# Kernel optimization log

Hardware: AMD Instinct MI355X
Metric: run time of the kernel (lower is better)

Reference implementation:

```python
import jax, jax.numpy as jnp
import numpy as np

NUM_HEADS = 12  # per-branch heads = NUM_HEADS // 3 = 4


def setup_inputs() -> dict:
    key = jax.random.key(0)
    ks = jax.random.split(key, 11)
    B, N, C = 4, 2048, 768
    s = 0.02
    return {
        "x": jax.random.normal(ks[0], (B, N, C), jnp.float32),
        "Wqkv1": jax.random.normal(ks[1], (C, C), jnp.float32) * s,
        "Wqkv2": jax.random.normal(ks[2], (C, C), jnp.float32) * s,
        "Wqkv3": jax.random.normal(ks[3], (C, C), jnp.float32) * s,
        "Wp1": jax.random.normal(ks[4], (C // 3, C), jnp.float32) * s,
        "bp1": jax.random.normal(ks[5], (C,), jnp.float32) * s,
        "Wp2": jax.random.normal(ks[6], (C // 3, C), jnp.float32) * s,
        "bp2": jax.random.normal(ks[7], (C,), jnp.float32) * s,
        "Wp3": jax.random.normal(ks[8], (C // 3, C), jnp.float32) * s,
        "bp3": jax.random.normal(ks[9], (C,), jnp.float32) * s,
        "Wg": jax.random.normal(ks[10], (C, 3), jnp.float32) * s,
    }


def _branch(x, Wqkv, Wp, bp, B, N, C):
    Hb = NUM_HEADS // 3          # heads per branch
    hd = C // NUM_HEADS          # head dim
    scale = hd ** (-0.5)
    qkv = (x @ Wqkv).reshape(B, N, 3, Hb, hd)
    qkv = jnp.transpose(qkv, (2, 0, 3, 1, 4))  # [3, B, Hb, N, hd]
    q, k, v = qkv[0], qkv[1], qkv[2]
    attn = jax.nn.softmax(jnp.einsum('bhqd,bhkd->bhqk', q, k) * scale, axis=-1)
    o = jnp.einsum('bhqk,bhkd->bqhd', attn, v).reshape(B, N, C // 3)
    return o @ Wp + bp  # [B, N, C]


def _gate(z, Wg):
    prob_soft = jax.nn.softmax(z @ Wg, axis=-1)
    prob_hard = jax.nn.one_hot(jnp.argmax(prob_soft, axis=-1), 3, dtype=prob_soft.dtype)
    # straight-through estimator
    return jax.lax.stop_gradient(prob_hard - prob_soft) + prob_soft


def reference(x, Wqkv1, Wqkv2, Wqkv3, Wp1, bp1, Wp2, bp2, Wp3, bp3, Wg):
    B, N, C = x.shape
    prob_true = _gate(x, Wg)                                # [B, N, 3]
    x1 = _branch(x, Wqkv1, Wp1, bp1, B, N, C)
    x2 = _branch(x, Wqkv2, Wp2, bp2, B, N, C)
    x3 = _branch(x, Wqkv3, Wp3, bp3, B, N, C)
    # detached gate path (gate sees stop_gradient(x))
    prob_true_d = _gate(jax.lax.stop_gradient(x), Wg)
    xo = (x1 * prob_true[..., 0:1] + x2 * prob_true[..., 1:2]
          + x3 * prob_true[..., 2:3])
    sg = jax.lax.stop_gradient
    xd = (sg(x1) * prob_true_d[..., 0:1] + sg(x2) * prob_true_d[..., 1:2]
          + sg(x3) * prob_true_d[..., 2:3])
    idx = jnp.argmax(prob_true, axis=-1).reshape(-1, 1)
    return (xo, xd, idx)
```

## Files before the change

kernel.cpp:

```cpp
#include <hip/hip_runtime.h>

typedef short s16x4 __attribute__((ext_vector_type(4)));
typedef short s16x8 __attribute__((ext_vector_type(8)));
typedef float f32x4 __attribute__((ext_vector_type(4)));
typedef unsigned u32x4 __attribute__((ext_vector_type(4)));
typedef unsigned short u16;
typedef unsigned char u8;

__device__ __forceinline__ u16 f2b(float f) {
    union { float f; unsigned u; } v; v.f = f;
    unsigned r = v.u + 0x7FFFu + ((v.u >> 16) & 1u);
    return (u16)(r >> 16);
}

__device__ __forceinline__ float fexp2(float x) {
    float r; asm("v_exp_f32 %0, %1" : "=v"(r) : "v"(x)); return r;
}

__device__ __forceinline__ unsigned cvtpk(float lo, float hi) {
    unsigned r; asm("v_cvt_pk_bf16_f32 %0, %1, %2" : "=v"(r) : "v"(lo), "v"(hi)); return r;
}

__device__ __forceinline__ void GLL(const void* g, void* l) {
    __builtin_amdgcn_global_load_lds(
        (const __attribute__((address_space(1))) unsigned int*)g,
        (__attribute__((address_space(3))) unsigned int*)l, 16, 0, 0);
}

__device__ __forceinline__ void vmwait0() {
    asm volatile("s_waitcnt vmcnt(0)" ::: "memory");
    __builtin_amdgcn_sched_barrier(0);
}

#define QSCALE 0.1803368801111244f

__global__ __launch_bounds__(256) void prolog_kernel(const float* __restrict__ x,
                                                     const float* __restrict__ Wg,
                                                     u16* __restrict__ xb,
                                                     u8* __restrict__ kArr,
                                                     float* __restrict__ out,
                                                     const float* __restrict__ W0,
                                                     const float* __restrict__ W1,
                                                     const float* __restrict__ W2,
                                                     const float* __restrict__ W3,
                                                     const float* __restrict__ W4,
                                                     const float* __restrict__ W5,
                                                     u16* __restrict__ wqt,
                                                     u16* __restrict__ wpt) {
    __shared__ u16 tile[32][34];
    if (blockIdx.x < 2048) {
        int t = blockIdx.x * 4 + (threadIdx.x >> 6);
        int lane = threadIdx.x & 63;
        const float* xr = x + (size_t)t * 768;
        u16* xw = xb + (size_t)t * 768;
        float z0 = 0.f, z1 = 0.f, z2 = 0.f;
        #pragma unroll
        for (int s = 0; s < 3; s++) {
            int base = s * 256 + lane * 4;
            f32x4 v = *(const f32x4*)(xr + base);
            s16x4 o;
            #pragma unroll
            for (int j = 0; j < 4; j++) {
                o[j] = (short)f2b(v[j]);
                z0 = fmaf(v[j], Wg[(base + j) * 3 + 0], z0);
                z1 = fmaf(v[j], Wg[(base + j) * 3 + 1], z1);
                z2 = fmaf(v[j], Wg[(base + j) * 3 + 2], z2);
            }
            *(s16x4*)(xw + base) = o;
        }
        for (int o = 32; o; o >>= 1) {
            z0 += __shfl_xor(z0, o);
            z1 += __shfl_xor(z1, o);
            z2 += __shfl_xor(z2, o);
        }
        if (lane == 0) {
            int k = 0; float b = z0;
            if (z1 > b) { b = z1; k = 1; }
            if (z2 > b) { b = z2; k = 2; }
            out[12582912 + t] = (float)k;
            kArr[t] = (u8)k;
        }
    } else {
        int wb = blockIdx.x - 2048;
        int y, bt;
        if (wb < 1728) { y = wb / 576; bt = wb % 576; }
        else           { int w2 = wb - 1728; y = 3 + w2 / 192; bt = w2 % 192; }
        const float* W; u16* dst; int K;
        if (y < 3) { W = (y == 0) ? W0 : (y == 1) ? W1 : W2; dst = wqt + y * 589824; K = 768; }
        else       { W = (y == 3) ? W3 : (y == 4) ? W4 : W5; dst = wpt + (y - 3) * 196608; K = 256; }
        int ktiles = K >> 5;
        int kt = bt % ktiles, nt = bt / ktiles;
        int tx = threadIdx.x & 31, ty = threadIdx.x >> 5;
        #pragma unroll
        for (int i = 0; i < 4; i++) {
            int k = kt * 32 + ty + i * 8;
            tile[ty + i * 8][tx] = f2b(W[(size_t)k * 768 + nt * 32 + tx]);
        }
        __syncthreads();
        #pragma unroll
        for (int i = 0; i < 4; i++) {
            int n = nt * 32 + ty + i * 8;
            dst[(size_t)n * K + kt * 32 + tx] = tile[tx][ty + i * 8];
        }
    }
}

__global__ __launch_bounds__(64) void compact_kernel(const u8* __restrict__ kArr,
                                                     u16* __restrict__ perm,
                                                     int* __restrict__ cnt,
                                                     int* __restrict__ startA) {
    int batch = blockIdx.x;
    int lane = threadIdx.x;
    const u8* ka = kArr + batch * 2048;
    u8 kv[32];
    #pragma unroll
    for (int i = 0; i < 32; i++) kv[i] = ka[i * 64 + lane];
    u16* pm = perm + batch * 2048;
    int off = 0;
    for (int br = 0; br < 3; br++) {
        int c = 0;
        #pragma unroll
        for (int i = 0; i < 32; i++) {
            bool p = (kv[i] == (u8)br);
            unsigned long long m = __ballot(p);
            int rank = __popcll(m & ((1ull << lane) - 1ull));
            if (p) pm[off + c + rank] = (u16)(i * 64 + lane);
            c += __popcll(m);
        }
        if (lane == 0) { cnt[br * 4 + batch] = c; startA[br * 4 + batch] = off; }
        off += c;
    }
}

__global__ __launch_bounds__(256) void qkv_gemm_kernel(const u16* __restrict__ A,
                                                       const u16* __restrict__ Bt_all,
                                                       const u16* __restrict__ perm,
                                                       const int* __restrict__ cnt,
                                                       const int* __restrict__ startA,
                                                       u16* __restrict__ Qo,
                                                       u16* __restrict__ Ko,
                                                       u16* __restrict__ Vt) {
    __shared__ u16 As[128 * 64];
    __shared__ u16 Bs[128 * 64];
    const int tid = threadIdx.x;
    const int lane = tid & 63, w = tid >> 6, wm = w >> 1, wn = w & 1;
    const int g = lane >> 4, c15 = lane & 15;
    const int cx = c15 & 7;
    const int b = blockIdx.x;
    const int j = b >> 3;
    const int v = j % 18;
    const int branch = v / 6;
    const int m0 = ((b & 7) * 8 + j / 18) * 128;
    const int n0 = (v % 6) * 128;
    const u16* Bt = Bt_all + (size_t)branch * 589824;

    const int l8 = lane >> 3;
    const int ch = (lane & 7) ^ l8;
    const int batch0 = m0 >> 11, pbase = m0 & 2047;
    const u16* Arow[4];
    if (n0 < 256) {
        const int cb = branch * 4 + batch0;
        const int count = min(2048, cnt[cb]);
        if (pbase >= count) return;
        const u16* ci = perm + batch0 * 2048 + startA[cb];
        #pragma unroll
        for (int it = 0; it < 4; it++) {
            int slot = pbase + w * 32 + l8 + it * 8;
            int tok = ci[slot < count ? slot : count - 1] & 2047;
            Arow[it] = A + (size_t)(batch0 * 2048 + tok) * 768 + ch * 8;
        }
    } else {
        #pragma unroll
        for (int it = 0; it < 4; it++)
            Arow[it] = A + (size_t)(m0 + w * 32 + l8 + it * 8) * 768 + ch * 8;
    }
    const u16* Bsrc = Bt + (size_t)(n0 + w * 32 + l8) * 768 + ch * 8;
    u16* AsW = As + w * 2048;
    u16* BsW = Bs + w * 2048;

    f32x4 z4 = {0.f, 0.f, 0.f, 0.f};
    f32x4 acc[4][4];
    for (int mi = 0; mi < 4; mi++)
        for (int ni = 0; ni < 4; ni++) acc[mi][ni] = z4;

    for (int k0 = 0; k0 < 768; k0 += 64) {
        __syncthreads();
        #pragma unroll
        for (int it = 0; it < 4; it++) {
            GLL(Arow[it] + k0, AsW + it * 512);
            GLL(Bsrc + (size_t)(it * 8) * 768 + k0, BsW + it * 512);
        }
        vmwait0();
        __syncthreads();
        #pragma unroll
        for (int kk = 0; kk < 2; kk++) {
            s16x8 af[4], bf[4];
            #pragma unroll
            for (int i = 0; i < 4; i++) {
                af[i] = *(const s16x8*)&As[(wm * 64 + i * 16 + c15) * 64 + (((kk * 4 + g) ^ cx) * 8)];
                bf[i] = *(const s16x8*)&Bs[(wn * 64 + i * 16 + c15) * 64 + (((kk * 4 + g) ^ cx) * 8)];
            }
            for (int mi = 0; mi < 4; mi++)
                for (int ni = 0; ni < 4; ni++)
                    acc[mi][ni] = __builtin_amdgcn_mfma_f32_16x16x32_bf16(
                        af[mi], bf[ni], acc[mi][ni], 0, 0, 0);
        }
    }

    for (int mi = 0; mi < 4; mi++) {
        int r = m0 + wm * 64 + mi * 16 + g * 4;
        int batch = r >> 11, nbase = r & 2047;
        for (int ni = 0; ni < 4; ni++) {
            int cN = n0 + wn * 64 + ni * 16 + c15;
            int p = cN >> 8, h = (cN >> 6) & 3, d = cN & 63;
            size_t hb = (size_t)((branch * 4 + batch) * 4 + h) * 131072;
            f32x4 vv = acc[mi][ni];
            if (p == 2) {
                s16x4 pk;
                for (int rg = 0; rg < 4; rg++) pk[rg] = (short)f2b(vv[rg]);
                int pos = nbase & 31;
                int slot = ((pos & 15) >> 2) * 8 + ((pos >> 4) << 2);
                *(s16x4*)(Vt + hb + (size_t)d * 2048 + (nbase & ~31) + slot) = pk;
            } else if (p == 0) {
                for (int rg = 0; rg < 4; rg++)
                    Qo[hb + (size_t)(nbase + rg) * 64 + d] = f2b(vv[rg] * QSCALE);
            } else {
                for (int rg = 0; rg < 4; rg++)
                    Ko[hb + (size_t)(nbase + rg) * 64 + d] = f2b(vv[rg]);
            }
        }
    }
}

#define ATTN_STEP(KF, VF) do {                                                              \
    _Pragma("unroll")                                                                       \
    for (int s = 0; s < 2; s++) {                                                           \
        f32x4 sa0 = __builtin_amdgcn_mfma_f32_16x16x32_bf16(KF[0][0], qf[s][0], z4, 0, 0, 0); \
        sa0 = __builtin_amdgcn_mfma_f32_16x16x32_bf16(KF[0][1], qf[s][1], sa0, 0, 0, 0);    \
        f32x4 sa1 = __builtin_amdgcn_mfma_f32_16x16x32_bf16(KF[1][0], qf[s][0], z4, 0, 0, 0); \
        sa1 = __builtin_amdgcn_mfma_f32_16x16x32_bf16(KF[1][1], qf[s][1], sa1, 0, 0, 0);    \
        float q0 = fexp2(sa0[0]), q1 = fexp2(sa0[1]);                                       \
        float q2 = fexp2(sa0[2]), q3 = fexp2(sa0[3]);                                       \
        float q4 = fexp2(sa1[0]), q5 = fexp2(sa1[1]);                                       \
        float q6 = fexp2(sa1[2]), q7 = fexp2(sa1[3]);                                       \
        lsp[s] += ((q0 + q1) + (q2 + q3)) + ((q4 + q5) + (q6 + q7));                        \
        u32x4 pw;                                                                           \
        pw[0] = cvtpk(q0, q1); pw[1] = cvtpk(q2, q3);                                       \
        pw[2] = cvtpk(q4, q5); pw[3] = cvtpk(q6, q7);                                       \
        union { u32x4 w; s16x8 h; } pu; pu.w = pw;                                          \
        s16x8 pb = pu.h;                                                                    \
        _Pragma("unroll")                                                                   \
        for (int dt = 0; dt < 4; dt++)                                                      \
            oac[s][dt] = __builtin_amdgcn_mfma_f32_16x16x32_bf16(VF[dt], pb, oac[s][dt], 0, 0, 0); \
    }                                                                                       \
} while (0)

#define STAGE(B, T) do {                                                  \
    const unsigned char* _ks = Ksrc + (size_t)(T) * 8192;                 \
    const unsigned char* _vs = Vsrc + (size_t)(T) * 128;                  \
    unsigned char* _kd = &lds[(B) * 16384 + w * 2048];                    \
    unsigned char* _vd = &lds[(B) * 16384 + 8192 + w * 2048];             \
    GLL(_ks, _kd); GLL(_ks + 1024, _kd + 1024);                           \
    GLL(_vs, _vd); GLL(_vs + 32768, _vd + 1024);                          \
} while (0)

#define TILE_STEP(B) do {                                                               \
    const unsigned char* _KL = &lds[(B) * 16384];                                       \
    const unsigned char* _VL = &lds[(B) * 16384 + 8192];                                \
    s16x8 kf[2][2], vf[4];                                                              \
    _Pragma("unroll")                                                                   \
    for (int t = 0; t < 2; t++)                                                         \
        _Pragma("unroll")                                                               \
        for (int h = 0; h < 2; h++)                                                     \
            kf[t][h] = *(const s16x8*)(_KL + (t * 16 + c) * 128 + (((h * 4 + g) ^ cx) * 16)); \
    _Pragma("unroll")                                                                   \
    for (int dt = 0; dt < 4; dt++)                                                      \
        vf[dt] = *(const s16x8*)(_VL + (dt * 16 + c) * 128 + ((g ^ cx) * 16));          \
    ATTN_STEP(kf, vf);                                                                  \
    _Pragma("unroll")                                                                   \
    for (int t = 0; t < 2; t++)                                                         \
        _Pragma("unroll")                                                               \
        for (int h = 0; h < 2; h++)                                                     \
            kf[t][h] = *(const s16x8*)(_KL + ((t + 2) * 16 + c) * 128 + (((h * 4 + g) ^ cx) * 16)); \
    _Pragma("unroll")                                                                   \
    for (int dt = 0; dt < 4; dt++)                                                      \
        vf[dt] = *(const s16x8*)(_VL + (dt * 16 + c) * 128 + (((4 + g) ^ cx) * 16));    \
    ATTN_STEP(kf, vf);                                                                  \
} while (0)

__global__ __launch_bounds__(256, 4) void attn_kernel(const u16* __restrict__ Qg,
                                                      const u16* __restrict__ Kg,
                                                      const u16* __restrict__ Vg,
                                                      const int* __restrict__ cnt,
                                                      u16* __restrict__ Og) {
    __shared__ unsigned char lds[32768];
    const int tid = threadIdx.x;
    const int w = tid >> 6, lane = tid & 63;
    const int b = blockIdx.x;
    const int j = b >> 3;
    const int inst = (b & 7) * 6 + (j % 6);
    const int branch = inst >> 4, batch = (inst >> 2) & 3, h = inst & 3;
    const int cb = branch * 4 + batch;
    const int count = min(2048, cnt[cb]);
    const int qbase = (j / 6) * 128;
    if (qbase >= count) return;
    const int qt = (j / 6) * 4 + w;
    const int g = lane >> 4, c = lane & 15;
    const int cx = c & 7;
    const u16* Qh = Qg + (size_t)inst * 131072;

    f32x4 z4 = {0.f, 0.f, 0.f, 0.f};
    s16x8 qf[2][2];
    #pragma unroll
    for (int kk = 0; kk < 2; kk++) {
        qf[0][kk] = *(const s16x8*)(Qh + (size_t)(qt * 32 + c) * 64 + kk * 32 + g * 8);
        qf[1][kk] = *(const s16x8*)(Qh + (size_t)(qt * 32 + 16 + c) * 64 + kk * 32 + g * 8);
    }

    f32x4 oac[2][4];
    #pragma unroll
    for (int s = 0; s < 2; s++)
        #pragma unroll
        for (int dt = 0; dt < 4; dt++) oac[s][dt] = z4;
    float lsp[2] = {0.f, 0.f};

    const int swz = (((lane & 7) ^ ((lane >> 3) & 7)) << 4);
    const unsigned char* Ksrc = (const unsigned char*)(Kg + (size_t)inst * 131072)
                                + w * 2048 + ((lane >> 3) << 7) + swz;
    const unsigned char* Vsrc = (const unsigned char*)(Vg + (size_t)inst * 131072)
                                + (size_t)w * 65536 + ((lane >> 3) << 12) + swz;

    STAGE(0, 0);
    vmwait0();
    __syncthreads();
    for (int t2 = 0; t2 < 32; t2++) {
        int cur = t2 & 1;
        if (t2 + 1 < 32) STAGE(cur ^ 1, t2 + 1);
        TILE_STEP(cur);
        vmwait0();
        __syncthreads();
    }

    #pragma unroll
    for (int s = 0; s < 2; s++) {
        float ls = lsp[s];
        ls += __shfl_xor(ls, 16);
        ls += __shfl_xor(ls, 32);
        float inv = 1.0f / ls;
        int slot = qt * 32 + s * 16 + c;
        u16* dst = Og + ((size_t)cb * 2048 + slot) * 256 + h * 64;
        #pragma unroll
        for (int dt = 0; dt < 4; dt++) {
            s16x4 ob;
            for (int rg = 0; rg < 4; rg++) ob[rg] = (short)f2b(oac[s][dt][rg] * inv);
            *(s16x4*)(dst + dt * 16 + g * 4) = ob;
        }
    }
}

__global__ __launch_bounds__(256) void proj_gemm_kernel(const u16* __restrict__ Oall,
                                                        const u16* __restrict__ Wpt_all,
                                                        const u16* __restrict__ perm,
                                                        const int* __restrict__ cnt,
                                                        const int* __restrict__ startA,
                                                        const float* __restrict__ bp1,
                                                        const float* __restrict__ bp2,
                                                        const float* __restrict__ bp3,
                                                        float* __restrict__ out) {
    __shared__ u16 As[128 * 64];
    __shared__ u16 Bs[128 * 64];
    const int tid = threadIdx.x;
    const int lane = tid & 63, w = tid >> 6, wm = w >> 1, wn = w & 1;
    const int g = lane >> 4, c15 = lane & 15;
    const int cx = c15 & 7;
    const int branch = blockIdx.z;
    const int m0 = blockIdx.y * 128, n0 = blockIdx.x * 128;
    const int batch = m0 >> 11;
    const int cb = branch * 4 + batch;
    const int count = min(2048, cnt[cb]);
    const int pbase = m0 & 2047;
    if (pbase >= count) return;
    const u16* A = Oall + (size_t)branch * 8192 * 256;
    const u16* Bt = Wpt_all + (size_t)branch * 196608;
    const float* bp = (branch == 0) ? bp1 : ((branch == 1) ? bp2 : bp3);

    const int l8 = lane >> 3;
    const int ch = (lane & 7) ^ l8;
    const u16* Asrc = A + (size_t)(m0 + w * 32 + l8) * 256 + ch * 8;
    const u16* Bsrc = Bt + (size_t)(n0 + w * 32 + l8) * 256 + ch * 8;
    u16* AsW = As + w * 2048;
    u16* BsW = Bs + w * 2048;

    f32x4 z4 = {0.f, 0.f, 0.f, 0.f};
    f32x4 acc[4][4];
    for (int mi = 0; mi < 4; mi++)
        for (int ni = 0; ni < 4; ni++) acc[mi][ni] = z4;

    for (int k0 = 0; k0 < 256; k0 += 64) {
        __syncthreads();
        #pragma unroll
        for (int it = 0; it < 4; it++) {
            GLL(Asrc + (size_t)(it * 8) * 256 + k0, AsW + it * 512);
            GLL(Bsrc + (size_t)(it * 8) * 256 + k0, BsW + it * 512);
        }
        vmwait0();
        __syncthreads();
        #pragma unroll
        for (int kk = 0; kk < 2; kk++) {
            s16x8 af[4], bf[4];
            #pragma unroll
            for (int i = 0; i < 4; i++) {
                af[i] = *(const s16x8*)&As[(wm * 64 + i * 16 + c15) * 64 + (((kk * 4 + g) ^ cx) * 8)];
                bf[i] = *(const s16x8*)&Bs[(wn * 64 + i * 16 + c15) * 64 + (((kk * 4 + g) ^ cx) * 8)];
            }
            for (int mi = 0; mi < 4; mi++)
                for (int ni = 0; ni < 4; ni++)
                    acc[mi][ni] = __builtin_amdgcn_mfma_f32_16x16x32_bf16(
                        af[mi], bf[ni], acc[mi][ni], 0, 0, 0);
        }
    }

    const u16* ci = perm + batch * 2048 + startA[cb];
    for (int mi = 0; mi < 4; mi++) {
        int r = pbase + wm * 64 + mi * 16 + g * 4;
        for (int ni = 0; ni < 4; ni++) {
            int cN = n0 + wn * 64 + ni * 16 + c15;
            float bj = bp[cN];
            f32x4 v = acc[mi][ni];
            for (int rg = 0; rg < 4; rg++) {
                int slot = r + rg;
                if (slot < count) {
                    int t = batch * 2048 + (ci[slot] & 2047);
                    float wv = v[rg] + bj;
                    out[(size_t)t * 768 + cN] = wv;
                    out[6291456u + (size_t)t * 768 + cN] = wv;
                }
            }
        }
    }
}

extern "C" void kernel_launch(void* const* d_in, const int* in_sizes, int n_in,
                              void* d_out, int out_size, void* d_ws, size_t ws_size,
                              hipStream_t stream) {
    const float* x   = (const float*)d_in[0];
    const float* Wq1 = (const float*)d_in[1];
    const float* Wq2 = (const float*)d_in[2];
    const float* Wq3 = (const float*)d_in[3];
    const float* Wp1 = (const float*)d_in[4];
    const float* bp1 = (const float*)d_in[5];
    const float* Wp2 = (const float*)d_in[6];
    const float* bp2 = (const float*)d_in[7];
    const float* Wp3 = (const float*)d_in[8];
    const float* bp3 = (const float*)d_in[9];
    const float* Wg  = (const float*)d_in[10];
    float* out = (float*)d_out;

    char* ws = (char*)d_ws;
    u16* xb    = (u16*)(ws + 0);
    u16* wqt   = (u16*)(ws + 12582912);
    u16* wpt   = (u16*)(ws + 16121856);
    u16* Qb    = (u16*)(ws + 17301504);
    u16* Kb    = (u16*)(ws + 29884416);
    u16* Vtb   = (u16*)(ws + 42467328);
    u16* Ob    = (u16*)(ws + 55050240);
    u16* perm  = (u16*)(ws + 67633152);
    int* cnt   = (int*)(ws + 67649536);
    int* start = (int*)(ws + 67649600);
    u8*  kArr  = (u8*) (ws + 67649664);

    prolog_kernel<<<4352, 256, 0, stream>>>(x, Wg, xb, kArr, out,
                                            Wq1, Wq2, Wq3, Wp1, Wp2, Wp3, wqt, wpt);
    compact_kernel<<<4, 64, 0, stream>>>(kArr, perm, cnt, start);
    qkv_gemm_kernel<<<1152, 256, 0, stream>>>(xb, wqt, perm, cnt, start, Qb, Kb, Vtb);
    attn_kernel<<<768, 256, 0, stream>>>(Qb, Kb, Vtb, cnt, Ob);
    proj_gemm_kernel<<<dim3(6, 64, 3), 256, 0, stream>>>(Ob, wpt, perm, cnt, start, bp1, bp2, bp3, out);
}
```

Baseline: 124.8 us.

## Double-buffer QKV GEMM LDS tiles with K-step 32 to overlap loads

The QKV projection GEMM now uses two LDS buffers with a K-slice of 32 instead of a single buffer with a K-slice of 64. The next slice is issued via global_load_lds before the MFMAs on the current one run, so memory latency overlaps compute. The LDS swizzle and per-lane source addressing are reworked for the 32-wide rows. This doubles the number of barriers and gives each stage less MFMA work to hide a load behind.

```diff
diff --git a/kernel.cpp b/kernel.cpp
--- a/kernel.cpp
+++ b/kernel.cpp
@@ -132,6 +132,13 @@
     }
 }
 
+#define QKV_STAGE(BUF, K0) do {                              \
+    GLL(srcA0 + (K0), &As[BUF][w * 1024]);                   \
+    GLL(srcA1 + (K0), &As[BUF][w * 1024 + 512]);             \
+    GLL(srcB0 + (K0), &Bs[BUF][w * 1024]);                   \
+    GLL(srcB1 + (K0), &Bs[BUF][w * 1024 + 512]);             \
+} while (0)
+
 __global__ __launch_bounds__(256) void qkv_gemm_kernel(const u16* __restrict__ A,
                                                        const u16* __restrict__ Bt_all,
                                                        const u16* __restrict__ perm,
@@ -140,12 +147,12 @@
                                                        u16* __restrict__ Qo,
                                                        u16* __restrict__ Ko,
                                                        u16* __restrict__ Vt) {
-    __shared__ u16 As[128 * 64];
-    __shared__ u16 Bs[128 * 64];
+    __shared__ u16 As[2][4096];
+    __shared__ u16 Bs[2][4096];
     const int tid = threadIdx.x;
     const int lane = tid & 63, w = tid >> 6, wm = w >> 1, wn = w & 1;
     const int g = lane >> 4, c15 = lane & 15;
-    const int cx = c15 & 7;
+    const int cx2 = c15 & 3;
     const int b = blockIdx.x;
     const int j = b >> 3;
     const int v = j % 18;
@@ -154,57 +161,51 @@
     const int n0 = (v % 6) * 128;
     const u16* Bt = Bt_all + (size_t)branch * 589824;
 
-    const int l8 = lane >> 3;
-    const int ch = (lane & 7) ^ l8;
+    const int l4 = lane >> 2;
+    const int ch = (lane & 3) ^ (l4 & 3);
     const int batch0 = m0 >> 11, pbase = m0 & 2047;
-    const u16* Arow[4];
+    const u16 *srcA0, *srcA1;
     if (n0 < 256) {
         const int cb = branch * 4 + batch0;
         const int count = min(2048, cnt[cb]);
         if (pbase >= count) return;
         const u16* ci = perm + batch0 * 2048 + startA[cb];
-        #pragma unroll
-        for (int it = 0; it < 4; it++) {
-            int slot = pbase + w * 32 + l8 + it * 8;
-            int tok = ci[slot < count ? slot : count - 1] & 2047;
-            Arow[it] = A + (size_t)(batch0 * 2048 + tok) * 768 + ch * 8;
-        }
+        int s0 = pbase + w * 32 + l4;      if (s0 >= count) s0 = count - 1;
+        int s1 = pbase + w * 32 + 16 + l4; if (s1 >= count) s1 = count - 1;
+        srcA0 = A + (size_t)(batch0 * 2048 + (ci[s0] & 2047)) * 768 + ch * 8;
+        srcA1 = A + (size_t)(batch0 * 2048 + (ci[s1] & 2047)) * 768 + ch * 8;
     } else {
-        #pragma unroll
-        for (int it = 0; it < 4; it++)
-            Arow[it] = A + (size_t)(m0 + w * 32 + l8 + it * 8) * 768 + ch * 8;
-    }
-    const u16* Bsrc = Bt + (size_t)(n0 + w * 32 + l8) * 768 + ch * 8;
-    u16* AsW = As + w * 2048;
-    u16* BsW = Bs + w * 2048;
+        srcA0 = A + (size_t)(m0 + w * 32 + l4) * 768 + ch * 8;
+        srcA1 = A + (size_t)(m0 + w * 32 + 16 + l4) * 768 + ch * 8;
+    }
+    const u16* srcB0 = Bt + (size_t)(n0 + w * 32 + l4) * 768 + ch * 8;
+    const u16* srcB1 = Bt + (size_t)(n0 + w * 32 + 16 + l4) * 768 + ch * 8;
 
     f32x4 z4 = {0.f, 0.f, 0.f, 0.f};
     f32x4 acc[4][4];
     for (int mi = 0; mi < 4; mi++)
         for (int ni = 0; ni < 4; ni++) acc[mi][ni] = z4;
 
-    for (int k0 = 0; k0 < 768; k0 += 64) {
-        __syncthreads();
-        #pragma unroll
-        for (int it = 0; it < 4; it++) {
-            GLL(Arow[it] + k0, AsW + it * 512);
-            GLL(Bsrc + (size_t)(it * 8) * 768 + k0, BsW + it * 512);
-        }
-        vmwait0();
-        __syncthreads();
-        #pragma unroll
-        for (int kk = 0; kk < 2; kk++) {
+    QKV_STAGE(0, 0);
+    vmwait0();
+    __syncthreads();
+    for (int st = 0; st < 24; st++) {
+        int cur = st & 1;
+        if (st + 1 < 24) QKV_STAGE(cur ^ 1, (st + 1) * 32);
+        {
             s16x8 af[4], bf[4];
             #pragma unroll
             for (int i = 0; i < 4; i++) {
-                af[i] = *(const s16x8*)&As[(wm * 64 + i * 16 + c15) * 64 + (((kk * 4 + g) ^ cx) * 8)];
-                bf[i] = *(const s16x8*)&Bs[(wn * 64 + i * 16 + c15) * 64 + (((kk * 4 + g) ^ cx) * 8)];
+                af[i] = *(const s16x8*)&As[cur][(wm * 64 + i * 16 + c15) * 32 + ((g ^ cx2) * 8)];
+                bf[i] = *(const s16x8*)&Bs[cur][(wn * 64 + i * 16 + c15) * 32 + ((g ^ cx2) * 8)];
             }
             for (int mi = 0; mi < 4; mi++)
                 for (int ni = 0; ni < 4; ni++)
                     acc[mi][ni] = __builtin_amdgcn_mfma_f32_16x16x32_bf16(
                         af[mi], bf[ni], acc[mi][ni], 0, 0, 0);
         }
+        vmwait0();
+        __syncthreads();
     }
 
     for (int mi = 0; mi < 4; mi++) {
```

New measurement: 125.1 us. About the same (+0.2%).
